# Kernel tuning notes

Hardware: AMD Instinct MI355X
Metric: run time of the kernel (lower is better)

## Reference

```python
import jax, jax.numpy as jnp
import numpy as np

B, T, K = 32, 8192, 16
EPS = 1e-7
LAM_FIRE, LAM_CANCEL, LAM_VALID, LAM_WRITE = 1.0, 1.0, 0.5, 0.5


def setup_inputs() -> dict:
    key = jax.random.key(0)
    ks = jax.random.split(key, 11)
    return {
        "trigger_hazard": jax.random.uniform(ks[0], (B, T, K), jnp.float32),
        "validity": jax.random.uniform(ks[1], (B, T, K), jnp.float32),
        "cancel_logits": jax.random.normal(ks[2], (B, T, K, 3), jnp.float32),
        "write_score": jax.random.normal(ks[3], (B, T, 1), jnp.float32),
        "live_mask": jax.random.randint(ks[4], (B, T, K), 0, 2).astype(bool),
        "contract_id": jax.random.randint(ks[5], (B, T, K), 0, 32),
        "oracle_fire": jax.random.randint(ks[6], (B, T, K), 0, 2).astype(jnp.float32),
        "oracle_cancel": jax.random.randint(ks[7], (B, T, K), 0, 4),
        "oracle_valid": jax.random.randint(ks[8], (B, T, K), 0, 2).astype(jnp.float32),
        "oracle_should_write": jax.random.randint(ks[9], (B, T, 1), 0, 2).astype(jnp.float32),
        "oracle_contract_id": jax.random.randint(ks[10], (B, T, K), 0, 32),
    }


def _masked_bce(p_raw, y, m):
    # Mirrors torch: BCE(clamp(p)*mask, y*mask), then *mask, sum / clamp(mask.sum(),1)
    n = jnp.maximum(m.sum(), 1.0)
    p = jnp.clip(p_raw, EPS, 1.0 - EPS) * m
    t = y * m
    # extra inner clip only guards masked entries (p==0), which are zeroed anyway
    bce = -(t * jnp.log(jnp.clip(p, EPS)) + (1.0 - t) * jnp.log(jnp.clip(1.0 - p, EPS)))
    return (bce * m).sum() / n


def _cancel_ce(logits, cancel_tgt, live_mask):
    has = ((cancel_tgt > 0) & live_mask).astype(jnp.float32)  # (B,T,K)
    n = has.sum()
    tgt = jnp.clip(cancel_tgt - 1, 0).astype(jnp.int32)
    logp = jax.nn.log_softmax(logits, axis=-1)  # (B,T,K,3)
    ce = -jnp.take_along_axis(logp, tgt[..., None], axis=-1)[..., 0]
    return jnp.where(n > 0, (ce * has).sum() / jnp.maximum(n, 1.0), 0.0)


def _bce_with_logits(x, y):
    return jnp.mean(jnp.maximum(x, 0.0) - x * y + jnp.log1p(jnp.exp(-jnp.abs(x))))


def reference(trigger_hazard, validity, cancel_logits, write_score, live_mask,
              contract_id, oracle_fire, oracle_cancel, oracle_valid,
              oracle_should_write, oracle_contract_id):
    # Vectorized align_oracle_to_model: broadcast compare + first-match argmax + gather
    match = (contract_id[..., :, None] == oracle_contract_id[..., None, :]) \
            & (contract_id != 0)[..., None]              # (B,T,Km,Ko)
    found = match.any(axis=-1)                           # (B,T,Km)
    idx = jnp.argmax(match, axis=-1)                     # first matching oracle slot

    def align_f(x):  # float tensors -> zeros where unmatched (torch out = zeros float)
        return jnp.where(found, jnp.take_along_axis(x, idx, axis=2), 0.0)

    fire_t = align_f(oracle_fire)
    valid_t = align_f(oracle_valid)
    cancel_t = jnp.where(found, jnp.take_along_axis(oracle_cancel, idx, axis=2), 0)

    m = live_mask.astype(jnp.float32)
    fire = LAM_FIRE * _masked_bce(trigger_hazard, fire_t, m)
    cancel = LAM_CANCEL * _cancel_ce(cancel_logits, cancel_t, live_mask)
    valid = LAM_VALID * _masked_bce(validity, valid_t, m)
    write = LAM_WRITE * _bce_with_logits(write_score, oracle_should_write)
    total = fire + cancel + valid + write
    return jnp.stack([fire, cancel, valid, write, total])
```

## Files before the change

kernel.cpp:

```cpp
#include <hip/hip_runtime.h>
#include <math.h>

#define EPS_F 1e-7f

constexpr int Bc = 32, Tc = 8192, Kc = 16;
constexpr int ROWS   = Bc * Tc;
constexpr int BLOCK  = 256;
constexpr int NITEM4 = ROWS * 4;
constexpr int NBLK   = NITEM4 / BLOCK;

typedef unsigned long long u64;

__device__ __forceinline__ u64 shflx64(u64 v, int m) {
  unsigned lo = __shfl_xor((unsigned)v, m, 64);
  unsigned hi = __shfl_xor((unsigned)(v >> 32), m, 64);
  return ((u64)hi << 32) | lo;
}

__global__ __launch_bounds__(BLOCK) void loss_main(
    const float* __restrict__ trig,
    const float* __restrict__ valp,
    const float* __restrict__ clog,
    const float* __restrict__ wscore,
    const int*   __restrict__ live,
    const int*   __restrict__ cid,
    const float* __restrict__ ofire,
    const int*   __restrict__ ocan,
    const float* __restrict__ ovalid,
    const float* __restrict__ oshw,
    const int*   __restrict__ ocid,
    float* __restrict__ part)
{
  const int tid  = threadIdx.x;
  const int lane = tid & 63;
  const int gi   = blockIdx.x * BLOCK + tid;
  const size_t o16 = (size_t)gi * 16;
  const size_t o48 = (size_t)gi * 48;

  const int4   oc = *(const int4*)  ((const char*)ocid   + o16);
  const int4   cc = *(const int4*)  ((const char*)ocan   + o16);
  const float4 ff = *(const float4*)((const char*)ofire  + o16);
  const float4 vv = *(const float4*)((const char*)ovalid + o16);
  const int4   cd = *(const int4*)  ((const char*)cid    + o16);
  const int4   lm = *(const int4*)  ((const char*)live   + o16);
  const float4 ph = *(const float4*)((const char*)trig   + o16);
  const float4 pq = *(const float4*)((const char*)valp   + o16);
  const float4 lA = *(const float4*)((const char*)clog   + o48 + 0);
  const float4 lB = *(const float4*)((const char*)clog   + o48 + 16);
  const float4 lC = *(const float4*)((const char*)clog   + o48 + 32);
  const int row = gi >> 2;
  const float wx = wscore[row];
  const float wy = oshw[row];

  u64 tblLo = 0ull, tblHi = 0ull, fndLo = 0ull, fndHi = 0ull;
  {
    const int   ocs[4] = {oc.x, oc.y, oc.z, oc.w};
    const int   ccs[4] = {cc.x, cc.y, cc.z, cc.w};
    const float ffs[4] = {ff.x, ff.y, ff.z, ff.w};
    const float vvs[4] = {vv.x, vv.y, vv.z, vv.w};
    #pragma unroll
    for (int j = 0; j < 4; ++j) {
      const unsigned c  = (unsigned)ocs[j] & 31u;
      const unsigned sh = (c & 15u) * 4u;
      const bool isLo   = c < 16u;
      const bool seen   = (((isLo ? fndLo : fndHi) >> sh) & 1ull) != 0ull;
      const unsigned nib = (unsigned)ffs[j] | ((unsigned)vvs[j] << 1) |
                           ((unsigned)ccs[j] << 2);
      const u64 add  = seen ? 0ull : ((u64)nib << sh);
      const u64 fadd = 0xFull << sh;
      tblLo |= isLo ? add : 0ull;
      tblHi |= isLo ? 0ull : add;
      fndLo |= isLo ? fadd : 0ull;
      fndHi |= isLo ? 0ull : fadd;
    }
  }

  #pragma unroll
  for (int m = 1; m <= 2; m <<= 1) {
    const u64 pTL = shflx64(tblLo, m);
    const u64 pTH = shflx64(tblHi, m);
    const u64 pFL = shflx64(fndLo, m);
    const u64 pFH = shflx64(fndHi, m);
    const bool iLow = (lane & m) == 0;
    const u64 loTL = iLow ? tblLo : pTL, hiTL = iLow ? pTL : tblLo;
    const u64 loTH = iLow ? tblHi : pTH, hiTH = iLow ? pTH : tblHi;
    const u64 loFL = iLow ? fndLo : pFL, hiFL = iLow ? pFL : fndLo;
    const u64 loFH = iLow ? fndHi : pFH, hiFH = iLow ? pFH : fndHi;
    tblLo = loTL | (hiTL & ~loFL);
    tblHi = loTH | (hiTH & ~loFH);
    fndLo = loFL | hiFL;
    fndHi = loFH | hiFH;
  }

  float a0 = 0.f, a1 = 0.f, a2 = 0.f, a3 = 0.f, a4 = 0.f;
  {
    const int   cds[4] = {cd.x, cd.y, cd.z, cd.w};
    const int   lms[4] = {lm.x, lm.y, lm.z, lm.w};
    const float phs[4] = {ph.x, ph.y, ph.z, ph.w};
    const float pqs[4] = {pq.x, pq.y, pq.z, pq.w};
    const float L0[4] = {lA.x, lA.w, lB.z, lC.y};
    const float L1[4] = {lA.y, lB.x, lB.w, lC.z};
    const float L2[4] = {lA.z, lB.y, lC.x, lC.w};
    #pragma unroll
    for (int j = 0; j < 4; ++j) {
      const unsigned c  = (unsigned)cds[j] & 31u;
      const unsigned sh = (c & 15u) * 4u;
      const bool isLo   = c < 16u;
      const bool fnd = (c != 0u) &&
                       ((((isLo ? fndLo : fndHi) >> sh) & 1ull) != 0ull);
      unsigned nib = (unsigned)(((isLo ? tblLo : tblHi) >> sh)) & 15u;
      nib = fnd ? nib : 0u;
      const float fire_t = (float)(nib & 1u);
      const float val_t  = (float)((nib >> 1) & 1u);
      const int   can_t  = (int)(nib >> 2);

      const float m = lms[j] ? 1.f : 0.f;

      const float p  = fminf(fmaxf(phs[j], EPS_F), 1.f - EPS_F);
      const float bf = -__logf((fire_t != 0.f) ? p : 1.f - p);
      const float q  = fminf(fmaxf(pqs[j], EPS_F), 1.f - EPS_F);
      const float bv = -__logf((val_t != 0.f) ? q : 1.f - q);

      const float has = (can_t > 0 && lms[j]) ? 1.f : 0.f;
      const int tgt = (can_t - 1) < 0 ? 0 : (can_t - 1);
      const float l0 = L0[j], l1 = L1[j], l2 = L2[j];
      const float mx  = fmaxf(l0, fmaxf(l1, l2));
      const float lse = mx + __logf(__expf(l0 - mx) + __expf(l1 - mx) +
                                    __expf(l2 - mx));
      const float lt  = (tgt == 0) ? l0 : ((tgt == 1) ? l1 : l2);

      a0 += bf * m;
      a1 += m;
      a2 += (lse - lt) * has;
      a3 += has;
      a4 += bv * m;
    }
  }

  float a5 = 0.f;
  if ((tid & 3) == 0) {
    a5 = fmaxf(wx, 0.f) - wx * wy + __logf(1.f + __expf(-fabsf(wx)));
  }

  float v[6] = {a0, a1, a2, a3, a4, a5};
  #pragma unroll
  for (int off = 32; off > 0; off >>= 1) {
    #pragma unroll
    for (int i = 0; i < 6; ++i) v[i] += __shfl_down(v[i], off, 64);
  }
  __shared__ float red[4][6];
  const int w = tid >> 6;
  if (lane == 0) {
    #pragma unroll
    for (int i = 0; i < 6; ++i) red[w][i] = v[i];
  }
  __syncthreads();
  if (tid == 0) {
    #pragma unroll
    for (int i = 0; i < 6; ++i)
      part[blockIdx.x * 6 + i] = red[0][i] + red[1][i] + red[2][i] + red[3][i];
  }
}

__global__ __launch_bounds__(BLOCK) void loss_finalize(
    const float* __restrict__ part, float* __restrict__ out)
{
  double v[6] = {0, 0, 0, 0, 0, 0};
  for (int r = threadIdx.x; r < NBLK; r += BLOCK) {
    #pragma unroll
    for (int i = 0; i < 6; ++i) v[i] += (double)part[r * 6 + i];
  }
  #pragma unroll
  for (int off = 32; off > 0; off >>= 1) {
    #pragma unroll
    for (int i = 0; i < 6; ++i) v[i] += __shfl_down(v[i], off, 64);
  }
  __shared__ double red[4][6];
  const int w = threadIdx.x >> 6, lane = threadIdx.x & 63;
  if (lane == 0) {
    #pragma unroll
    for (int i = 0; i < 6; ++i) red[w][i] = v[i];
  }
  __syncthreads();
  if (threadIdx.x == 0) {
    double a[6];
    #pragma unroll
    for (int i = 0; i < 6; ++i) a[i] = red[0][i] + red[1][i] + red[2][i] + red[3][i];
    const double live_n = a[1] < 1.0 ? 1.0 : a[1];
    const double fire   = a[0] / live_n;
    const double cancel = (a[3] > 0.0) ? a[2] / (a[3] < 1.0 ? 1.0 : a[3])
                                       : 0.0;
    const double valid  = 0.5 * a[4] / live_n;
    const double wr     = 0.5 * a[5] / (double)ROWS;
    out[0] = (float)fire;
    out[1] = (float)cancel;
    out[2] = (float)valid;
    out[3] = (float)wr;
    out[4] = (float)(fire + cancel + valid + wr);
  }
}

extern "C" void kernel_launch(void* const* d_in, const int* in_sizes, int n_in,
                              void* d_out, int out_size, void* d_ws, size_t ws_size,
                              hipStream_t stream) {
  const float* trig   = (const float*)d_in[0];
  const float* valp   = (const float*)d_in[1];
  const float* clog   = (const float*)d_in[2];
  const float* wscore = (const float*)d_in[3];
  const int*   live   = (const int*)  d_in[4];
  const int*   cid    = (const int*)  d_in[5];
  const float* ofire  = (const float*)d_in[6];
  const int*   ocan   = (const int*)  d_in[7];
  const float* ovalid = (const float*)d_in[8];
  const float* oshw   = (const float*)d_in[9];
  const int*   ocid   = (const int*)  d_in[10];
  float* out  = (float*)d_out;
  float* part = (float*)d_ws;

  loss_main<<<NBLK, BLOCK, 0, stream>>>(trig, valp, clog, wscore, live, cid,
                                        ofire, ocan, ovalid, oshw, ocid, part);
  loss_finalize<<<1, BLOCK, 0, stream>>>(part, out);
}
```

Baseline: 212.1 us.

## Process four tiles per thread with double-buffered register loads

Each block now handles four 256-thread tiles instead of one. Loads for the next tile are issued before computing the current one, using two register buffers, so memory latency overlaps with compute. This also cuts the block count fourfold, which reduces per-block reduction and partial-sum work. The cost is higher register pressure, which may lower occupancy.

```diff
diff --git a/kernel.cpp b/kernel.cpp
--- a/kernel.cpp
+++ b/kernel.cpp
@@ -7,7 +7,8 @@
 constexpr int ROWS   = Bc * Tc;
 constexpr int BLOCK  = 256;
 constexpr int NITEM4 = ROWS * 4;
-constexpr int NBLK   = NITEM4 / BLOCK;
+constexpr int UNROLL = 4;
+constexpr int NBLK   = NITEM4 / (BLOCK * UNROLL);
 
 typedef unsigned long long u64;
 
@@ -15,6 +16,129 @@
   unsigned lo = __shfl_xor((unsigned)v, m, 64);
   unsigned hi = __shfl_xor((unsigned)(v >> 32), m, 64);
   return ((u64)hi << 32) | lo;
+}
+
+struct Tile {
+  int4   oc, cc, cd, lm;
+  float4 ff, vv, ph, pq, lA, lB, lC;
+  float  wx, wy;
+};
+
+struct Ptrs {
+  const char *trig, *valp, *clog, *wscore, *live, *cid;
+  const char *ofire, *ocan, *ovalid, *oshw, *ocid;
+};
+
+__device__ __forceinline__ void load_tile(Tile& T, const Ptrs& P, int gi) {
+  const size_t o16 = (size_t)gi * 16;
+  const size_t o48 = (size_t)gi * 48;
+  T.oc = *(const int4*)  (P.ocid   + o16);
+  T.cc = *(const int4*)  (P.ocan   + o16);
+  T.ff = *(const float4*)(P.ofire  + o16);
+  T.vv = *(const float4*)(P.ovalid + o16);
+  T.cd = *(const int4*)  (P.cid    + o16);
+  T.lm = *(const int4*)  (P.live   + o16);
+  T.ph = *(const float4*)(P.trig   + o16);
+  T.pq = *(const float4*)(P.valp   + o16);
+  T.lA = *(const float4*)(P.clog   + o48 + 0);
+  T.lB = *(const float4*)(P.clog   + o48 + 16);
+  T.lC = *(const float4*)(P.clog   + o48 + 32);
+  const size_t ro = (size_t)(gi >> 2) * 4;
+  T.wx = *(const float*)(P.wscore + ro);
+  T.wy = *(const float*)(P.oshw   + ro);
+}
+
+__device__ __forceinline__ void compute_tile(
+    const Tile& T, int tid, int lane, float a[6])
+{
+  u64 tblLo = 0ull, tblHi = 0ull, fndLo = 0ull, fndHi = 0ull;
+  {
+    const int   ocs[4] = {T.oc.x, T.oc.y, T.oc.z, T.oc.w};
+    const int   ccs[4] = {T.cc.x, T.cc.y, T.cc.z, T.cc.w};
+    const float ffs[4] = {T.ff.x, T.ff.y, T.ff.z, T.ff.w};
+    const float vvs[4] = {T.vv.x, T.vv.y, T.vv.z, T.vv.w};
+    #pragma unroll
+    for (int j = 0; j < 4; ++j) {
+      const unsigned c  = (unsigned)ocs[j] & 31u;
+      const unsigned sh = (c & 15u) * 4u;
+      const bool isLo   = c < 16u;
+      const bool seen   = (((isLo ? fndLo : fndHi) >> sh) & 1ull) != 0ull;
+      const unsigned nib = (unsigned)ffs[j] | ((unsigned)vvs[j] << 1) |
+                           ((unsigned)ccs[j] << 2);
+      const u64 add  = seen ? 0ull : ((u64)nib << sh);
+      const u64 fadd = 0xFull << sh;
+      tblLo |= isLo ? add : 0ull;
+      tblHi |= isLo ? 0ull : add;
+      fndLo |= isLo ? fadd : 0ull;
+      fndHi |= isLo ? 0ull : fadd;
+    }
+  }
+
+  #pragma unroll
+  for (int m = 1; m <= 2; m <<= 1) {
+    const u64 pTL = shflx64(tblLo, m);
+    const u64 pTH = shflx64(tblHi, m);
+    const u64 pFL = shflx64(fndLo, m);
+    const u64 pFH = shflx64(fndHi, m);
+    const bool iLow = (lane & m) == 0;
+    const u64 loTL = iLow ? tblLo : pTL, hiTL = iLow ? pTL : tblLo;
+    const u64 loTH = iLow ? tblHi : pTH, hiTH = iLow ? pTH : tblHi;
+    const u64 loFL = iLow ? fndLo : pFL, hiFL = iLow ? pFL : fndLo;
+    const u64 loFH = iLow ? fndHi : pFH, hiFH = iLow ? pFH : fndHi;
+    tblLo = loTL | (hiTL & ~loFL);
+    tblHi = loTH | (hiTH & ~loFH);
+    fndLo = loFL | hiFL;
+    fndHi = loFH | hiFH;
+  }
+
+  {
+    const int   cds[4] = {T.cd.x, T.cd.y, T.cd.z, T.cd.w};
+    const int   lms[4] = {T.lm.x, T.lm.y, T.lm.z, T.lm.w};
+    const float phs[4] = {T.ph.x, T.ph.y, T.ph.z, T.ph.w};
+    const float pqs[4] = {T.pq.x, T.pq.y, T.pq.z, T.pq.w};
+    const float L0[4] = {T.lA.x, T.lA.w, T.lB.z, T.lC.y};
+    const float L1[4] = {T.lA.y, T.lB.x, T.lB.w, T.lC.z};
+    const float L2[4] = {T.lA.z, T.lB.y, T.lC.x, T.lC.w};
+    #pragma unroll
+    for (int j = 0; j < 4; ++j) {
+      const unsigned c  = (unsigned)cds[j] & 31u;
+      const unsigned sh = (c & 15u) * 4u;
+      const bool isLo   = c < 16u;
+      const bool fnd = (c != 0u) &&
+                       ((((isLo ? fndLo : fndHi) >> sh) & 1ull) != 0ull);
+      unsigned nib = (unsigned)(((isLo ? tblLo : tblHi) >> sh)) & 15u;
+      nib = fnd ? nib : 0u;
+      const float fire_t = (float)(nib & 1u);
+      const float val_t  = (float)((nib >> 1) & 1u);
+      const int   can_t  = (int)(nib >> 2);
+
+      const float m = lms[j] ? 1.f : 0.f;
+
+      const float p  = fminf(fmaxf(phs[j], EPS_F), 1.f - EPS_F);
+      const float bf = -__logf((fire_t != 0.f) ? p : 1.f - p);
+      const float q  = fminf(fmaxf(pqs[j], EPS_F), 1.f - EPS_F);
+      const float bv = -__logf((val_t != 0.f) ? q : 1.f - q);
+
+      const float has = (can_t > 0 && lms[j]) ? 1.f : 0.f;
+      const int tgt = (can_t - 1) < 0 ? 0 : (can_t - 1);
+      const float l0 = L0[j], l1 = L1[j], l2 = L2[j];
+      const float mx  = fmaxf(l0, fmaxf(l1, l2));
+      const float lse = mx + __logf(__expf(l0 - mx) + __expf(l1 - mx) +
+                                    __expf(l2 - mx));
+      const float lt  = (tgt == 0) ? l0 : ((tgt == 1) ? l1 : l2);
+
+      a[0] += bf * m;
+      a[1] += m;
+      a[2] += (lse - lt) * has;
+      a[3] += has;
+      a[4] += bv * m;
+    }
+  }
+
+  if ((tid & 3) == 0) {
+    a[5] += fmaxf(T.wx, 0.f) - T.wx * T.wy +
+            __logf(1.f + __expf(-fabsf(T.wx)));
+  }
 }
 
 __global__ __launch_bounds__(BLOCK) void loss_main(
@@ -33,126 +157,38 @@
 {
   const int tid  = threadIdx.x;
   const int lane = tid & 63;
-  const int gi   = blockIdx.x * BLOCK + tid;
-  const size_t o16 = (size_t)gi * 16;
-  const size_t o48 = (size_t)gi * 48;
-
-  const int4   oc = *(const int4*)  ((const char*)ocid   + o16);
-  const int4   cc = *(const int4*)  ((const char*)ocan   + o16);
-  const float4 ff = *(const float4*)((const char*)ofire  + o16);
-  const float4 vv = *(const float4*)((const char*)ovalid + o16);
-  const int4   cd = *(const int4*)  ((const char*)cid    + o16);
-  const int4   lm = *(const int4*)  ((const char*)live   + o16);
-  const float4 ph = *(const float4*)((const char*)trig   + o16);
-  const float4 pq = *(const float4*)((const char*)valp   + o16);
-  const float4 lA = *(const float4*)((const char*)clog   + o48 + 0);
-  const float4 lB = *(const float4*)((const char*)clog   + o48 + 16);
-  const float4 lC = *(const float4*)((const char*)clog   + o48 + 32);
-  const int row = gi >> 2;
-  const float wx = wscore[row];
-  const float wy = oshw[row];
-
-  u64 tblLo = 0ull, tblHi = 0ull, fndLo = 0ull, fndHi = 0ull;
-  {
-    const int   ocs[4] = {oc.x, oc.y, oc.z, oc.w};
-    const int   ccs[4] = {cc.x, cc.y, cc.z, cc.w};
-    const float ffs[4] = {ff.x, ff.y, ff.z, ff.w};
-    const float vvs[4] = {vv.x, vv.y, vv.z, vv.w};
-    #pragma unroll
-    for (int j = 0; j < 4; ++j) {
-      const unsigned c  = (unsigned)ocs[j] & 31u;
-      const unsigned sh = (c & 15u) * 4u;
-      const bool isLo   = c < 16u;
-      const bool seen   = (((isLo ? fndLo : fndHi) >> sh) & 1ull) != 0ull;
-      const unsigned nib = (unsigned)ffs[j] | ((unsigned)vvs[j] << 1) |
-                           ((unsigned)ccs[j] << 2);
-      const u64 add  = seen ? 0ull : ((u64)nib << sh);
-      const u64 fadd = 0xFull << sh;
-      tblLo |= isLo ? add : 0ull;
-      tblHi |= isLo ? 0ull : add;
-      fndLo |= isLo ? fadd : 0ull;
-      fndHi |= isLo ? 0ull : fadd;
-    }
-  }
-
-  #pragma unroll
-  for (int m = 1; m <= 2; m <<= 1) {
-    const u64 pTL = shflx64(tblLo, m);
-    const u64 pTH = shflx64(tblHi, m);
-    const u64 pFL = shflx64(fndLo, m);
-    const u64 pFH = shflx64(fndHi, m);
-    const bool iLow = (lane & m) == 0;
-    const u64 loTL = iLow ? tblLo : pTL, hiTL = iLow ? pTL : tblLo;
-    const u64 loTH = iLow ? tblHi : pTH, hiTH = iLow ? pTH : tblHi;
-    const u64 loFL = iLow ? fndLo : pFL, hiFL = iLow ? pFL : fndLo;
-    const u64 loFH = iLow ? fndHi : pFH, hiFH = iLow ? pFH : fndHi;
-    tblLo = loTL | (hiTL & ~loFL);
-    tblHi = loTH | (hiTH & ~loFH);
-    fndLo = loFL | hiFL;
-    fndHi = loFH | hiFH;
-  }
-
-  float a0 = 0.f, a1 = 0.f, a2 = 0.f, a3 = 0.f, a4 = 0.f;
-  {
-    const int   cds[4] = {cd.x, cd.y, cd.z, cd.w};
-    const int   lms[4] = {lm.x, lm.y, lm.z, lm.w};
-    const float phs[4] = {ph.x, ph.y, ph.z, ph.w};
-    const float pqs[4] = {pq.x, pq.y, pq.z, pq.w};
-    const float L0[4] = {lA.x, lA.w, lB.z, lC.y};
-    const float L1[4] = {lA.y, lB.x, lB.w, lC.z};
-    const float L2[4] = {lA.z, lB.y, lC.x, lC.w};
-    #pragma unroll
-    for (int j = 0; j < 4; ++j) {
-      const unsigned c  = (unsigned)cds[j] & 31u;
-      const unsigned sh = (c & 15u) * 4u;
-      const bool isLo   = c < 16u;
-      const bool fnd = (c != 0u) &&
-                       ((((isLo ? fndLo : fndHi) >> sh) & 1ull) != 0ull);
-      unsigned nib = (unsigned)(((isLo ? tblLo : tblHi) >> sh)) & 15u;
-      nib = fnd ? nib : 0u;
-      const float fire_t = (float)(nib & 1u);
-      const float val_t  = (float)((nib >> 1) & 1u);
-      const int   can_t  = (int)(nib >> 2);
-
-      const float m = lms[j] ? 1.f : 0.f;
-
-      const float p  = fminf(fmaxf(phs[j], EPS_F), 1.f - EPS_F);
-      const float bf = -__logf((fire_t != 0.f) ? p : 1.f - p);
-      const float q  = fminf(fmaxf(pqs[j], EPS_F), 1.f - EPS_F);
-      const float bv = -__logf((val_t != 0.f) ? q : 1.f - q);
-
-      const float has = (can_t > 0 && lms[j]) ? 1.f : 0.f;
-      const int tgt = (can_t - 1) < 0 ? 0 : (can_t - 1);
-      const float l0 = L0[j], l1 = L1[j], l2 = L2[j];
-      const float mx  = fmaxf(l0, fmaxf(l1, l2));
-      const float lse = mx + __logf(__expf(l0 - mx) + __expf(l1 - mx) +
-                                    __expf(l2 - mx));
-      const float lt  = (tgt == 0) ? l0 : ((tgt == 1) ? l1 : l2);
-
-      a0 += bf * m;
-      a1 += m;
-      a2 += (lse - lt) * has;
-      a3 += has;
-      a4 += bv * m;
-    }
-  }
-
-  float a5 = 0.f;
-  if ((tid & 3) == 0) {
-    a5 = fmaxf(wx, 0.f) - wx * wy + __logf(1.f + __expf(-fabsf(wx)));
-  }
-
-  float v[6] = {a0, a1, a2, a3, a4, a5};
+  const int gi0  = blockIdx.x * (BLOCK * UNROLL) + tid;
+
+  Ptrs P;
+  P.trig = (const char*)trig;   P.valp   = (const char*)valp;
+  P.clog = (const char*)clog;   P.wscore = (const char*)wscore;
+  P.live = (const char*)live;   P.cid    = (const char*)cid;
+  P.ofire= (const char*)ofire;  P.ocan   = (const char*)ocan;
+  P.ovalid=(const char*)ovalid; P.oshw   = (const char*)oshw;
+  P.ocid = (const char*)ocid;
+
+  float a[6] = {0.f, 0.f, 0.f, 0.f, 0.f, 0.f};
+
+  Tile A, B;
+  load_tile(A, P, gi0 + 0 * BLOCK);
+  load_tile(B, P, gi0 + 1 * BLOCK);
+  compute_tile(A, tid, lane, a);
+  load_tile(A, P, gi0 + 2 * BLOCK);
+  compute_tile(B, tid, lane, a);
+  load_tile(B, P, gi0 + 3 * BLOCK);
+  compute_tile(A, tid, lane, a);
+  compute_tile(B, tid, lane, a);
+
   #pragma unroll
   for (int off = 32; off > 0; off >>= 1) {
     #pragma unroll
-    for (int i = 0; i < 6; ++i) v[i] += __shfl_down(v[i], off, 64);
+    for (int i = 0; i < 6; ++i) a[i] += __shfl_down(a[i], off, 64);
   }
   __shared__ float red[4][6];
   const int w = tid >> 6;
   if (lane == 0) {
     #pragma unroll
-    for (int i = 0; i < 6; ++i) red[w][i] = v[i];
+    for (int i = 0; i < 6; ++i) red[w][i] = a[i];
   }
   __syncthreads();
   if (tid == 0) {
```

Measured after the change: 211.1 us. No clear change (-0.5%).

## Use persistent blocks with double-buffered global-to-LDS async loads

Applied to the files above, without the earlier changes.

Replaces one-item-per-thread blocks with 512 persistent blocks that loop over stages. Each stage streams eight 16-byte-per-item arrays into a double-buffered LDS region using global_load_lds, waiting on vmcnt so the next stage's loads overlap the current stage's compute. The intent is to hide memory latency and cut launch and per-block reduction overhead. It adds 64KB of LDS per block, which limits occupancy. The hand-placed waitcnt synchronization without a block barrier is fragile, since each wave reads only its own lanes' data.

```diff
diff --git a/kernel.cpp b/kernel.cpp
--- a/kernel.cpp
+++ b/kernel.cpp
@@ -4,10 +4,16 @@
 #define EPS_F 1e-7f
 
 constexpr int Bc = 32, Tc = 8192, Kc = 16;
-constexpr int ROWS   = Bc * Tc;
-constexpr int BLOCK  = 256;
-constexpr int NITEM4 = ROWS * 4;
-constexpr int NBLK   = NITEM4 / BLOCK;
+constexpr int ROWS     = Bc * Tc;
+constexpr int BLOCK    = 256;
+constexpr int NITEM4   = ROWS * 4;
+constexpr int ST_ITEMS = 512;
+constexpr int NST      = NITEM4 / ST_ITEMS;
+constexpr int NBLK     = 512;
+constexpr int ST_PER_BLK = NST / NBLK;
+constexpr int REG_B    = ST_ITEMS * 16;
+constexpr int NARR     = 8;
+constexpr int BUF_B    = NARR * REG_B;
 
 typedef unsigned long long u64;
 
@@ -15,6 +21,146 @@
   unsigned lo = __shfl_xor((unsigned)v, m, 64);
   unsigned hi = __shfl_xor((unsigned)(v >> 32), m, 64);
   return ((u64)hi << 32) | lo;
+}
+
+__device__ __forceinline__ void dma16(void* lds, const void* g) {
+  __builtin_amdgcn_global_load_lds(
+      (const __attribute__((address_space(1))) void*)g,
+      (__attribute__((address_space(3))) void*)lds, 16, 0, 0);
+}
+
+#define WAITCNT_VM(N)                                                      \
+  do {                                                                     \
+    asm volatile("s_waitcnt vmcnt(" #N ")" ::: "memory");                  \
+    __builtin_amdgcn_sched_barrier(0);                                     \
+  } while (0)
+
+struct Ptrs {
+  const char* a16[NARR];
+  const char* clog;
+  const char* wscore;
+  const char* oshw;
+};
+
+__device__ __forceinline__ void stage(char* buf, const Ptrs& P, int T,
+                                      int w, int lane) {
+  #pragma unroll
+  for (int a = 0; a < NARR; ++a) {
+    const char* g = P.a16[a];
+    char* r = buf + a * REG_B + w * 1024;
+    dma16(r + 0 * 4096, g + (size_t)(T + 0 * 256 + w * 64 + lane) * 16);
+    dma16(r + 1 * 4096, g + (size_t)(T + 1 * 256 + w * 64 + lane) * 16);
+  }
+}
+
+__device__ __forceinline__ void compute_item(
+    const char* buf, int u, int tid, int lane, int gi, const Ptrs& P,
+    float a[6])
+{
+  const int ib = u * 4096 + tid * 16;
+  const int4   oc = *(const int4*)  (buf + 0 * REG_B + ib);
+  const int4   cc = *(const int4*)  (buf + 1 * REG_B + ib);
+  const float4 ff = *(const float4*)(buf + 2 * REG_B + ib);
+  const float4 vv = *(const float4*)(buf + 3 * REG_B + ib);
+  const int4   cd = *(const int4*)  (buf + 4 * REG_B + ib);
+  const int4   lm = *(const int4*)  (buf + 5 * REG_B + ib);
+  const float4 ph = *(const float4*)(buf + 6 * REG_B + ib);
+  const float4 pq = *(const float4*)(buf + 7 * REG_B + ib);
+  const size_t o48 = (size_t)gi * 48;
+  const float4 lA = *(const float4*)(P.clog + o48 + 0);
+  const float4 lB = *(const float4*)(P.clog + o48 + 16);
+  const float4 lC = *(const float4*)(P.clog + o48 + 32);
+  const int row = gi >> 2;
+  const float wx = *(const float*)(P.wscore + (size_t)row * 4);
+  const float wy = *(const float*)(P.oshw   + (size_t)row * 4);
+
+  u64 tblLo = 0ull, tblHi = 0ull, fndLo = 0ull, fndHi = 0ull;
+  {
+    const int   ocs[4] = {oc.x, oc.y, oc.z, oc.w};
+    const int   ccs[4] = {cc.x, cc.y, cc.z, cc.w};
+    const float ffs[4] = {ff.x, ff.y, ff.z, ff.w};
+    const float vvs[4] = {vv.x, vv.y, vv.z, vv.w};
+    #pragma unroll
+    for (int j = 0; j < 4; ++j) {
+      const unsigned c  = (unsigned)ocs[j] & 31u;
+      const unsigned sh = (c & 15u) * 4u;
+      const bool isLo   = c < 16u;
+      const bool seen   = (((isLo ? fndLo : fndHi) >> sh) & 1ull) != 0ull;
+      const unsigned nib = (unsigned)ffs[j] | ((unsigned)vvs[j] << 1) |
+                           ((unsigned)ccs[j] << 2);
+      const u64 add  = seen ? 0ull : ((u64)nib << sh);
+      const u64 fadd = 0xFull << sh;
+      tblLo |= isLo ? add : 0ull;
+      tblHi |= isLo ? 0ull : add;
+      fndLo |= isLo ? fadd : 0ull;
+      fndHi |= isLo ? 0ull : fadd;
+    }
+  }
+
+  #pragma unroll
+  for (int m = 1; m <= 2; m <<= 1) {
+    const u64 pTL = shflx64(tblLo, m);
+    const u64 pTH = shflx64(tblHi, m);
+    const u64 pFL = shflx64(fndLo, m);
+    const u64 pFH = shflx64(fndHi, m);
+    const bool iLow = (lane & m) == 0;
+    const u64 loTL = iLow ? tblLo : pTL, hiTL = iLow ? pTL : tblLo;
+    const u64 loTH = iLow ? tblHi : pTH, hiTH = iLow ? pTH : tblHi;
+    const u64 loFL = iLow ? fndLo : pFL, hiFL = iLow ? pFL : fndLo;
+    const u64 loFH = iLow ? fndHi : pFH, hiFH = iLow ? pFH : fndHi;
+    tblLo = loTL | (hiTL & ~loFL);
+    tblHi = loTH | (hiTH & ~loFH);
+    fndLo = loFL | hiFL;
+    fndHi = loFH | hiFH;
+  }
+
+  {
+    const int   cds[4] = {cd.x, cd.y, cd.z, cd.w};
+    const int   lms[4] = {lm.x, lm.y, lm.z, lm.w};
+    const float phs[4] = {ph.x, ph.y, ph.z, ph.w};
+    const float pqs[4] = {pq.x, pq.y, pq.z, pq.w};
+    const float L0[4] = {lA.x, lA.w, lB.z, lC.y};
+    const float L1[4] = {lA.y, lB.x, lB.w, lC.z};
+    const float L2[4] = {lA.z, lB.y, lC.x, lC.w};
+    #pragma unroll
+    for (int j = 0; j < 4; ++j) {
+      const unsigned c  = (unsigned)cds[j] & 31u;
+      const unsigned sh = (c & 15u) * 4u;
+      const bool isLo   = c < 16u;
+      const bool fnd = (c != 0u) &&
+                       ((((isLo ? fndLo : fndHi) >> sh) & 1ull) != 0ull);
+      unsigned nib = (unsigned)(((isLo ? tblLo : tblHi) >> sh)) & 15u;
+      nib = fnd ? nib : 0u;
+      const float fire_t = (float)(nib & 1u);
+      const float val_t  = (float)((nib >> 1) & 1u);
+      const int   can_t  = (int)(nib >> 2);
+
+      const float m = lms[j] ? 1.f : 0.f;
+
+      const float p  = fminf(fmaxf(phs[j], EPS_F), 1.f - EPS_F);
+      const float bf = -__logf((fire_t != 0.f) ? p : 1.f - p);
+      const float q  = fminf(fmaxf(pqs[j], EPS_F), 1.f - EPS_F);
+      const float bv = -__logf((val_t != 0.f) ? q : 1.f - q);
+
+      const float has = (can_t > 0 && lms[j]) ? 1.f : 0.f;
+      const int tgt = (can_t - 1) < 0 ? 0 : (can_t - 1);
+      const float l0 = L0[j], l1 = L1[j], l2 = L2[j];
+      const float mx  = fmaxf(l0, fmaxf(l1, l2));
+      const float lse = mx + __logf(__expf(l0 - mx) + __expf(l1 - mx) +
+                                    __expf(l2 - mx));
+      const float lt  = (tgt == 0) ? l0 : ((tgt == 1) ? l1 : l2);
+
+      a[0] += bf * m;
+      a[1] += m;
+      a[2] += (lse - lt) * has;
+      a[3] += has;
+      a[4] += bv * m;
+    }
+  }
+
+  if ((tid & 3) == 0) {
+    a[5] += fmaxf(wx, 0.f) - wx * wy + __logf(1.f + __expf(-fabsf(wx)));
+  }
 }
 
 __global__ __launch_bounds__(BLOCK) void loss_main(
@@ -31,128 +177,49 @@
     const int*   __restrict__ ocid,
     float* __restrict__ part)
 {
+  __shared__ __align__(16) char smem[2 * BUF_B];
+
   const int tid  = threadIdx.x;
   const int lane = tid & 63;
-  const int gi   = blockIdx.x * BLOCK + tid;
-  const size_t o16 = (size_t)gi * 16;
-  const size_t o48 = (size_t)gi * 48;
-
-  const int4   oc = *(const int4*)  ((const char*)ocid   + o16);
-  const int4   cc = *(const int4*)  ((const char*)ocan   + o16);
-  const float4 ff = *(const float4*)((const char*)ofire  + o16);
-  const float4 vv = *(const float4*)((const char*)ovalid + o16);
-  const int4   cd = *(const int4*)  ((const char*)cid    + o16);
-  const int4   lm = *(const int4*)  ((const char*)live   + o16);
-  const float4 ph = *(const float4*)((const char*)trig   + o16);
-  const float4 pq = *(const float4*)((const char*)valp   + o16);
-  const float4 lA = *(const float4*)((const char*)clog   + o48 + 0);
-  const float4 lB = *(const float4*)((const char*)clog   + o48 + 16);
-  const float4 lC = *(const float4*)((const char*)clog   + o48 + 32);
-  const int row = gi >> 2;
-  const float wx = wscore[row];
-  const float wy = oshw[row];
-
-  u64 tblLo = 0ull, tblHi = 0ull, fndLo = 0ull, fndHi = 0ull;
-  {
-    const int   ocs[4] = {oc.x, oc.y, oc.z, oc.w};
-    const int   ccs[4] = {cc.x, cc.y, cc.z, cc.w};
-    const float ffs[4] = {ff.x, ff.y, ff.z, ff.w};
-    const float vvs[4] = {vv.x, vv.y, vv.z, vv.w};
-    #pragma unroll
-    for (int j = 0; j < 4; ++j) {
-      const unsigned c  = (unsigned)ocs[j] & 31u;
-      const unsigned sh = (c & 15u) * 4u;
-      const bool isLo   = c < 16u;
-      const bool seen   = (((isLo ? fndLo : fndHi) >> sh) & 1ull) != 0ull;
-      const unsigned nib = (unsigned)ffs[j] | ((unsigned)vvs[j] << 1) |
-                           ((unsigned)ccs[j] << 2);
-      const u64 add  = seen ? 0ull : ((u64)nib << sh);
-      const u64 fadd = 0xFull << sh;
-      tblLo |= isLo ? add : 0ull;
-      tblHi |= isLo ? 0ull : add;
-      fndLo |= isLo ? fadd : 0ull;
-      fndHi |= isLo ? 0ull : fadd;
+  const int w    = tid >> 6;
+  const int T0   = blockIdx.x * (ST_PER_BLK * ST_ITEMS);
+
+  Ptrs P;
+  P.a16[0] = (const char*)ocid;  P.a16[1] = (const char*)ocan;
+  P.a16[2] = (const char*)ofire; P.a16[3] = (const char*)ovalid;
+  P.a16[4] = (const char*)cid;   P.a16[5] = (const char*)live;
+  P.a16[6] = (const char*)trig;  P.a16[7] = (const char*)valp;
+  P.clog   = (const char*)clog;
+  P.wscore = (const char*)wscore;
+  P.oshw   = (const char*)oshw;
+
+  float a[6] = {0.f, 0.f, 0.f, 0.f, 0.f, 0.f};
+
+  stage(smem, P, T0, w, lane);
+
+  for (int s = 0; s < ST_PER_BLK; ++s) {
+    char* buf = smem + (s & 1) * BUF_B;
+    if (s + 1 < ST_PER_BLK) {
+      asm volatile("s_waitcnt lgkmcnt(0)" ::: "memory");
+      stage(smem + ((s + 1) & 1) * BUF_B, P, T0 + (s + 1) * ST_ITEMS, w, lane);
+      WAITCNT_VM(16);
+    } else {
+      WAITCNT_VM(0);
     }
-  }
-
-  #pragma unroll
-  for (int m = 1; m <= 2; m <<= 1) {
-    const u64 pTL = shflx64(tblLo, m);
-    const u64 pTH = shflx64(tblHi, m);
-    const u64 pFL = shflx64(fndLo, m);
-    const u64 pFH = shflx64(fndHi, m);
-    const bool iLow = (lane & m) == 0;
-    const u64 loTL = iLow ? tblLo : pTL, hiTL = iLow ? pTL : tblLo;
-    const u64 loTH = iLow ? tblHi : pTH, hiTH = iLow ? pTH : tblHi;
-    const u64 loFL = iLow ? fndLo : pFL, hiFL = iLow ? pFL : fndLo;
-    const u64 loFH = iLow ? fndHi : pFH, hiFH = iLow ? pFH : fndHi;
-    tblLo = loTL | (hiTL & ~loFL);
-    tblHi = loTH | (hiTH & ~loFH);
-    fndLo = loFL | hiFL;
-    fndHi = loFH | hiFH;
-  }
-
-  float a0 = 0.f, a1 = 0.f, a2 = 0.f, a3 = 0.f, a4 = 0.f;
-  {
-    const int   cds[4] = {cd.x, cd.y, cd.z, cd.w};
-    const int   lms[4] = {lm.x, lm.y, lm.z, lm.w};
-    const float phs[4] = {ph.x, ph.y, ph.z, ph.w};
-    const float pqs[4] = {pq.x, pq.y, pq.z, pq.w};
-    const float L0[4] = {lA.x, lA.w, lB.z, lC.y};
-    const float L1[4] = {lA.y, lB.x, lB.w, lC.z};
-    const float L2[4] = {lA.z, lB.y, lC.x, lC.w};
-    #pragma unroll
-    for (int j = 0; j < 4; ++j) {
-      const unsigned c  = (unsigned)cds[j] & 31u;
-      const unsigned sh = (c & 15u) * 4u;
-      const bool isLo   = c < 16u;
-      const bool fnd = (c != 0u) &&
-                       ((((isLo ? fndLo : fndHi) >> sh) & 1ull) != 0ull);
-      unsigned nib = (unsigned)(((isLo ? tblLo : tblHi) >> sh)) & 15u;
-      nib = fnd ? nib : 0u;
-      const float fire_t = (float)(nib & 1u);
-      const float val_t  = (float)((nib >> 1) & 1u);
-      const int   can_t  = (int)(nib >> 2);
-
-      const float m = lms[j] ? 1.f : 0.f;
-
-      const float p  = fminf(fmaxf(phs[j], EPS_F), 1.f - EPS_F);
-      const float bf = -__logf((fire_t != 0.f) ? p : 1.f - p);
-      const float q  = fminf(fmaxf(pqs[j], EPS_F), 1.f - EPS_F);
-      const float bv = -__logf((val_t != 0.f) ? q : 1.f - q);
-
-      const float has = (can_t > 0 && lms[j]) ? 1.f : 0.f;
-      const int tgt = (can_t - 1) < 0 ? 0 : (can_t - 1);
-      const float l0 = L0[j], l1 = L1[j], l2 = L2[j];
-      const float mx  = fmaxf(l0, fmaxf(l1, l2));
-      const float lse = mx + __logf(__expf(l0 - mx) + __expf(l1 - mx) +
-                                    __expf(l2 - mx));
-      const float lt  = (tgt == 0) ? l0 : ((tgt == 1) ? l1 : l2);
-
-      a0 += bf * m;
-      a1 += m;
-      a2 += (lse - lt) * has;
-      a3 += has;
-      a4 += bv * m;
-    }
-  }
-
-  float a5 = 0.f;
-  if ((tid & 3) == 0) {
-    a5 = fmaxf(wx, 0.f) - wx * wy + __logf(1.f + __expf(-fabsf(wx)));
-  }
-
-  float v[6] = {a0, a1, a2, a3, a4, a5};
+    const int T = T0 + s * ST_ITEMS;
+    compute_item(buf, 0, tid, lane, T + 0 * 256 + tid, P, a);
+    compute_item(buf, 1, tid, lane, T + 1 * 256 + tid, P, a);
+  }
+
   #pragma unroll
   for (int off = 32; off > 0; off >>= 1) {
     #pragma unroll
-    for (int i = 0; i < 6; ++i) v[i] += __shfl_down(v[i], off, 64);
+    for (int i = 0; i < 6; ++i) a[i] += __shfl_down(a[i], off, 64);
   }
   __shared__ float red[4][6];
-  const int w = tid >> 6;
   if (lane == 0) {
     #pragma unroll
-    for (int i = 0; i < 6; ++i) red[w][i] = v[i];
+    for (int i = 0; i < 6; ++i) red[w][i] = a[i];
   }
   __syncthreads();
   if (tid == 0) {
```

New measurement: 218.8 us. 1.03x slower.
